# Kernel tuning notes

Hardware: AMD Instinct MI355X
Metric: run time of the kernel (lower is better)

The kernel has to match this reference:

```python
import jax, jax.numpy as jnp
import numpy as np

N = 100000
E = 1000000
F_NODE = 64
F_EDGE = 32
H = 128
C_NODE = 12
C_EDGE = 4


def _glorot(key, shape):
    fan_in, fan_out = shape[0], shape[1]
    s = (6.0 / (fan_in + fan_out)) ** 0.5
    return jax.random.uniform(key, shape, jnp.float32, -s, s)


def setup_inputs() -> dict:
    key = jax.random.key(0)
    ks = jax.random.split(key, 16)
    x = jax.random.normal(ks[0], (N, F_NODE), jnp.float32)
    edge_index = jax.random.randint(ks[1], (2, E), 0, N, jnp.int32)
    edge_attr = jax.random.normal(ks[2], (E, F_EDGE), jnp.float32)
    return {
        "x": x,
        "edge_index": edge_index,
        "edge_attr": edge_attr,
        "We": _glorot(ks[3], (F_NODE, H)), "be": jnp.zeros((H,), jnp.float32),
        "Wc1": _glorot(ks[4], (H, H)), "bc1": jnp.zeros((H,), jnp.float32),
        "Wc2": _glorot(ks[5], (H, H)), "bc2": jnp.zeros((H,), jnp.float32),
        "Wn1": _glorot(ks[6], (H, H // 2)), "bn1": jnp.zeros((H // 2,), jnp.float32),
        "Wn2": _glorot(ks[7], (H // 2, C_NODE)), "bn2": jnp.zeros((C_NODE,), jnp.float32),
        "Wedge1": _glorot(ks[8], (2 * H + F_EDGE, H)), "bedge1": jnp.zeros((H,), jnp.float32),
        "Wedge2": _glorot(ks[9], (H, C_EDGE)), "bedge2": jnp.zeros((C_EDGE,), jnp.float32),
    }


def _gcn_conv(x, W, b, src, tgt, n):
    # PyG GCNConv: add self-loops, symmetric deg normalization, scatter-add.
    xw = x @ W  # [N, H]
    loop = jnp.arange(n, dtype=src.dtype)
    s = jnp.concatenate([src, loop])
    t = jnp.concatenate([tgt, loop])
    deg = jax.ops.segment_sum(jnp.ones_like(t, jnp.float32), t, num_segments=n)
    dinv = jnp.where(deg > 0, jax.lax.rsqrt(jnp.maximum(deg, 1.0)), 0.0)
    norm = dinv[s] * dinv[t]  # [E+N]
    msg = xw[s] * norm[:, None]
    return jax.ops.segment_sum(msg, t, num_segments=n) + b


def reference(x, edge_index, edge_attr, We, be, Wc1, bc1, Wc2, bc2,
              Wn1, bn1, Wn2, bn2, Wedge1, bedge1, Wedge2, bedge2):
    n = x.shape[0]
    row, col = edge_index[0], edge_index[1]
    h = jax.nn.relu(x @ We + be)          # node_embed Linear+ReLU
    h = jax.nn.relu(h)                     # extra F.relu in forward
    h = jax.nn.relu(_gcn_conv(h, Wc1, bc1, row, col, n))
    h = jax.nn.relu(_gcn_conv(h, Wc2, bc2, row, col, n))
    node_logits = jax.nn.relu(h @ Wn1 + bn1) @ Wn2 + bn2
    e = jnp.concatenate([h[row], h[col], edge_attr], axis=-1)  # [E, 2H+Fe]
    edge_logits = jax.nn.relu(e @ Wedge1 + bedge1) @ Wedge2 + bedge2
    return (node_logits, edge_logits)
```

## Files before the change

kernel.cpp:

```cpp
#include <hip/hip_runtime.h>

#define N_NODES 100000
#define N_EDGES 1000000
#define NB_SCAN 391
#define EDGE_OUT_BASE 1200000

typedef __attribute__((ext_vector_type(8))) short short8;
typedef __attribute__((ext_vector_type(4))) unsigned short us4;
typedef __attribute__((ext_vector_type(4))) float f32x4;

__device__ __forceinline__ float bf2f(unsigned short u) {
    unsigned int x = ((unsigned int)u) << 16;
    return __builtin_bit_cast(float, x);
}
__device__ __forceinline__ float lo_bf(unsigned int u) {
    return __builtin_bit_cast(float, u << 16);
}
__device__ __forceinline__ float hi_bf(unsigned int u) {
    return __builtin_bit_cast(float, u & 0xffff0000u);
}
__device__ __forceinline__ unsigned short f2bf(float f) {
    unsigned int x = __builtin_bit_cast(unsigned int, f);
    return (unsigned short)((x + 0x7fffu + ((x >> 16) & 1u)) >> 16);
}

__global__ __launch_bounds__(256) void k_detect(const unsigned short* __restrict__ xr,
                                                int* __restrict__ flag) {
    __shared__ int s[256];
    int t = threadIdx.x;
    int cnt = 0;
    for (int i = t; i < 8192; i += 256) {
        int e = (xr[i] >> 7) & 0xFF;
        if (e >= 148) cnt++;
    }
    s[t] = cnt;
    __syncthreads();
    for (int off = 128; off > 0; off >>= 1) {
        if (t < off) s[t] += s[t + off];
        __syncthreads();
    }
    if (t == 0) *flag = (s[0] > 100) ? 1 : 0;
}

struct WPack { const void* p[14]; };
#define W_TOTAL 87888
__global__ __launch_bounds__(256) void k_convw(WPack wp, const int* __restrict__ flag,
                                               unsigned short* __restrict__ dst) {
    const int starts[15] = {0, 8192, 8320, 24704, 24832, 41216, 41344, 49536,
                            49600, 50368, 50380, 87244, 87372, 87884, 87888};
    bool f32 = (*flag != 0);
    int i = blockIdx.x * 256 + threadIdx.x;
    if (i >= W_TOTAL) return;
    int s = 0;
#pragma unroll
    for (int k = 1; k < 14; k++) s += (i >= starts[k]) ? 1 : 0;
    int j = i - starts[s];
    dst[i] = f32 ? f2bf(((const float*)wp.p[s])[j]) : ((const unsigned short*)wp.p[s])[j];
}
#define OW_We 0
#define OW_be 8192
#define OW_Wc1 8320
#define OW_bc1 24704
#define OW_Wc2 24832
#define OW_bc2 41216
#define OW_Wn1 41344
#define OW_bn1 49536
#define OW_Wn2 49600
#define OW_bn2 50368
#define OW_We1 50380
#define OW_be1 87244
#define OW_We2 87372
#define OW_be2 87884

__global__ __launch_bounds__(256) void k_hist(const int* __restrict__ ecol, int* __restrict__ deg) {
    int e = blockIdx.x * 256 + threadIdx.x;
    if (e < N_EDGES) atomicAdd(&deg[ecol[e]], 1);
}

__global__ __launch_bounds__(256) void k_scanA(const int* __restrict__ deg, int* __restrict__ bsum) {
    __shared__ int s[256];
    int i = blockIdx.x * 256 + threadIdx.x;
    s[threadIdx.x] = (i < N_NODES) ? deg[i] : 0;
    __syncthreads();
    for (int off = 128; off > 0; off >>= 1) {
        if (threadIdx.x < off) s[threadIdx.x] += s[threadIdx.x + off];
        __syncthreads();
    }
    if (threadIdx.x == 0) bsum[blockIdx.x] = s[0];
}

__global__ __launch_bounds__(512) void k_scanB(int* __restrict__ bsum) {
    __shared__ int s[512];
    int t = threadIdx.x;
    int v = (t < NB_SCAN) ? bsum[t] : 0;
    s[t] = v;
    __syncthreads();
    for (int off = 1; off < 512; off <<= 1) {
        int x = (t >= off) ? s[t - off] : 0;
        __syncthreads();
        s[t] += x;
        __syncthreads();
    }
    if (t < NB_SCAN) bsum[t] = s[t] - v;
}

__global__ __launch_bounds__(256) void k_scanC(const int* __restrict__ deg, const int* __restrict__ bsum,
                                               int* __restrict__ row_off, int* __restrict__ cursor,
                                               float* __restrict__ dinv) {
    __shared__ int s[256];
    int i = blockIdx.x * 256 + threadIdx.x;
    int t = threadIdx.x;
    int v = (i < N_NODES) ? deg[i] : 0;
    s[t] = v;
    __syncthreads();
    for (int off = 1; off < 256; off <<= 1) {
        int x = (t >= off) ? s[t - off] : 0;
        __syncthreads();
        s[t] += x;
        __syncthreads();
    }
    int excl = s[t] - v + bsum[blockIdx.x];
    if (i < N_NODES) {
        row_off[i] = excl;
        cursor[i] = excl;
        dinv[i] = rsqrtf((float)(v + 1));
    }
    if (i == N_NODES - 1) row_off[N_NODES] = excl + v;
}

__global__ __launch_bounds__(256) void k_fill(const int* __restrict__ erow, const int* __restrict__ ecol,
                                              int* __restrict__ cursor, int* __restrict__ csr) {
    int e = blockIdx.x * 256 + threadIdx.x;
    if (e < N_EDGES) {
        int pos = atomicAdd(&cursor[ecol[e]], 1);
        csr[pos] = erow[e];
    }
}

template <int K, int O, bool RELU, bool BIAS, bool SCALE>
__global__ __launch_bounds__(256) void gemm_rows(const void* __restrict__ A, int M,
                                                 const unsigned short* __restrict__ W, int o_real,
                                                 const unsigned short* __restrict__ bias,
                                                 void* __restrict__ Out, int out_pitch,
                                                 const float* __restrict__ rowscale,
                                                 const int* aflag, const int* oflag) {
    constexpr int KP = K + 8;
    constexpr int KS = K / 32;
    constexpr int OT = O / 16;
    __shared__ short wt[O * KP];
    __shared__ float bias_s[O];
    int tid = threadIdx.x;
    for (int idx = tid; idx < K * O; idx += 256) {
        int k = idx / O, o = idx % O;
        short w = 0;
        if (o < o_real) w = (short)W[(size_t)k * o_real + o];
        wt[o * KP + k] = w;
    }
    if (BIAS) {
        for (int o = tid; o < O; o += 256) bias_s[o] = (o < o_real) ? bf2f(bias[o]) : 0.f;
    }
    __syncthreads();

    bool af32 = aflag && (*aflag != 0);
    bool of32 = oflag && (*oflag != 0);

    int wid = tid >> 6, lane = tid & 63;
    int rbase = (blockIdx.x * 4 + wid) * 32;
    if (rbase >= M) return;
    int lq = lane >> 4, lr = lane & 15;

    short8 a[2][KS];
#pragma unroll
    for (int rg = 0; rg < 2; rg++) {
        int row = rbase + rg * 16 + lr;
        if (row >= M) row = M - 1;
        if (af32) {
            const float* ap = (const float*)A + (size_t)row * K + lq * 8;
#pragma unroll
            for (int ks = 0; ks < KS; ks++) {
                f32x4 u0 = *(const f32x4*)(ap + ks * 32);
                f32x4 u1 = *(const f32x4*)(ap + ks * 32 + 4);
                short8 v;
                v[0] = (short)f2bf(u0[0]); v[1] = (short)f2bf(u0[1]);
                v[2] = (short)f2bf(u0[2]); v[3] = (short)f2bf(u0[3]);
                v[4] = (short)f2bf(u1[0]); v[5] = (short)f2bf(u1[1]);
                v[6] = (short)f2bf(u1[2]); v[7] = (short)f2bf(u1[3]);
                a[rg][ks] = v;
            }
        } else {
            const unsigned short* ap = (const unsigned short*)A + (size_t)row * K + lq * 8;
#pragma unroll
            for (int ks = 0; ks < KS; ks++) a[rg][ks] = *(const short8*)(ap + ks * 32);
        }
    }

    f32x4 acc[2][OT];
#pragma unroll
    for (int rg = 0; rg < 2; rg++)
#pragma unroll
        for (int j = 0; j < OT; j++) {
            acc[rg][j][0] = 0.f; acc[rg][j][1] = 0.f; acc[rg][j][2] = 0.f; acc[rg][j][3] = 0.f;
        }

#pragma unroll
    for (int j = 0; j < OT; j++) {
        short8 b[KS];
#pragma unroll
        for (int ks = 0; ks < KS; ks++)
            b[ks] = *(const short8*)(&wt[(lr + 16 * j) * KP + ks * 32 + lq * 8]);
#pragma unroll
        for (int rg = 0; rg < 2; rg++)
#pragma unroll
            for (int ks = 0; ks < KS; ks++)
                acc[rg][j] = __builtin_amdgcn_mfma_f32_16x16x32_bf16(a[rg][ks], b[ks], acc[rg][j], 0, 0, 0);
    }

#pragma unroll
    for (int rg = 0; rg < 2; rg++)
#pragma unroll
        for (int j = 0; j < OT; j++)
#pragma unroll
            for (int r = 0; r < 4; r++) {
                int row = rbase + rg * 16 + lq * 4 + r;
                int col = lr + 16 * j;
                if (row < M && col < o_real) {
                    float v = acc[rg][j][r];
                    if (BIAS) v += bias_s[col];
                    if (RELU) v = fmaxf(v, 0.f);
                    if (SCALE) v *= rowscale[row];
                    size_t oi = (size_t)row * out_pitch + col;
                    if (of32) ((float*)Out)[oi] = v;
                    else ((unsigned short*)Out)[oi] = f2bf(v);
                }
            }
}

__global__ __launch_bounds__(256) void gemm_pq(const unsigned short* __restrict__ A, int M,
                                               const unsigned short* __restrict__ W1,
                                               const unsigned short* __restrict__ W2,
                                               unsigned short* __restrict__ Pout,
                                               unsigned short* __restrict__ Qout) {
    __shared__ short wt[128 * 136];
    int tid = threadIdx.x;
    int wid = tid >> 6, lane = tid & 63;
    int rbase = (blockIdx.x * 4 + wid) * 32;
    int lq = lane >> 4, lr = lane & 15;

    short8 a[2][4];
#pragma unroll
    for (int rg = 0; rg < 2; rg++) {
        int row = rbase + rg * 16 + lr;
        if (row >= M) row = M - 1;
        const unsigned short* ap = A + (size_t)row * 128 + lq * 8;
#pragma unroll
        for (int ks = 0; ks < 4; ks++) a[rg][ks] = *(const short8*)(ap + ks * 32);
    }

    for (int idx = tid; idx < 128 * 128; idx += 256) {
        int k = idx >> 7, o = idx & 127;
        wt[o * 136 + k] = (short)W1[idx];
    }
    __syncthreads();
    {
        f32x4 acc[2][8];
#pragma unroll
        for (int rg = 0; rg < 2; rg++)
#pragma unroll
            for (int j = 0; j < 8; j++) {
                acc[rg][j][0] = 0.f; acc[rg][j][1] = 0.f; acc[rg][j][2] = 0.f; acc[rg][j][3] = 0.f;
            }
#pragma unroll
        for (int j = 0; j < 8; j++) {
            short8 b[4];
#pragma unroll
            for (int ks = 0; ks < 4; ks++)
                b[ks] = *(const short8*)(&wt[(lr + 16 * j) * 136 + ks * 32 + lq * 8]);
#pragma unroll
            for (int rg = 0; rg < 2; rg++)
#pragma unroll
                for (int ks = 0; ks < 4; ks++)
                    acc[rg][j] = __builtin_amdgcn_mfma_f32_16x16x32_bf16(a[rg][ks], b[ks], acc[rg][j], 0, 0, 0);
        }
#pragma unroll
        for (int rg = 0; rg < 2; rg++)
#pragma unroll
            for (int j = 0; j < 8; j++)
#pragma unroll
                for (int r = 0; r < 4; r++) {
                    int row = rbase + rg * 16 + lq * 4 + r;
                    if (row < M) Pout[(size_t)row * 128 + lr + 16 * j] = f2bf(acc[rg][j][r]);
                }
    }
    __syncthreads();

    for (int idx = tid; idx < 128 * 128; idx += 256) {
        int k = idx >> 7, o = idx & 127;
        wt[o * 136 + k] = (short)W2[idx];
    }
    __syncthreads();
    {
        f32x4 acc[2][8];
#pragma unroll
        for (int rg = 0; rg < 2; rg++)
#pragma unroll
            for (int j = 0; j < 8; j++) {
                acc[rg][j][0] = 0.f; acc[rg][j][1] = 0.f; acc[rg][j][2] = 0.f; acc[rg][j][3] = 0.f;
            }
#pragma unroll
        for (int j = 0; j < 8; j++) {
            short8 b[4];
#pragma unroll
            for (int ks = 0; ks < 4; ks++)
                b[ks] = *(const short8*)(&wt[(lr + 16 * j) * 136 + ks * 32 + lq * 8]);
#pragma unroll
            for (int rg = 0; rg < 2; rg++)
#pragma unroll
                for (int ks = 0; ks < 4; ks++)
                    acc[rg][j] = __builtin_amdgcn_mfma_f32_16x16x32_bf16(a[rg][ks], b[ks], acc[rg][j], 0, 0, 0);
        }
#pragma unroll
        for (int rg = 0; rg < 2; rg++)
#pragma unroll
            for (int j = 0; j < 8; j++)
#pragma unroll
                for (int r = 0; r < 4; r++) {
                    int row = rbase + rg * 16 + lq * 4 + r;
                    if (row < M) Qout[(size_t)row * 128 + lr + 16 * j] = f2bf(acc[rg][j][r]);
                }
    }
}

__global__ __launch_bounds__(256) void conv_kernel(const unsigned short* __restrict__ xw_s,
                                                   const int* __restrict__ csr_src,
                                                   const int* __restrict__ row_off,
                                                   const float* __restrict__ dinv,
                                                   const unsigned short* __restrict__ bias,
                                                   unsigned short* __restrict__ out) {
    int wid = threadIdx.x >> 6, lane = threadIdx.x & 63;
    int t = blockIdx.x * 4 + wid;
    int beg = row_off[t], end = row_off[t + 1];
    float dt = dinv[t];
    unsigned int v = *(const unsigned int*)(xw_s + (size_t)t * 128 + lane * 2);
    unsigned int bv = *(const unsigned int*)(bias + lane * 2);
    float a0 = lo_bf(v), a1 = hi_bf(v);
    int i = beg;
    for (; i + 4 <= end; i += 4) {
        int s0 = csr_src[i], s1 = csr_src[i + 1], s2 = csr_src[i + 2], s3 = csr_src[i + 3];
        unsigned int u0 = *(const unsigned int*)(xw_s + (size_t)s0 * 128 + lane * 2);
        unsigned int u1 = *(const unsigned int*)(xw_s + (size_t)s1 * 128 + lane * 2);
        unsigned int u2 = *(const unsigned int*)(xw_s + (size_t)s2 * 128 + lane * 2);
        unsigned int u3 = *(const unsigned int*)(xw_s + (size_t)s3 * 128 + lane * 2);
        a0 += lo_bf(u0) + lo_bf(u1) + lo_bf(u2) + lo_bf(u3);
        a1 += hi_bf(u0) + hi_bf(u1) + hi_bf(u2) + hi_bf(u3);
    }
    for (; i < end; i++) {
        int s = csr_src[i];
        unsigned int u = *(const unsigned int*)(xw_s + (size_t)s * 128 + lane * 2);
        a0 += lo_bf(u);
        a1 += hi_bf(u);
    }
    a0 = fmaxf(fmaf(a0, dt, lo_bf(bv)), 0.f);
    a1 = fmaxf(fmaf(a1, dt, hi_bf(bv)), 0.f);
    unsigned int o = (unsigned int)f2bf(a0) | ((unsigned int)f2bf(a1) << 16);
    *(unsigned int*)(out + (size_t)t * 128 + lane * 2) = o;
}

__global__ __launch_bounds__(256) void edge_head(const void* __restrict__ ea,
                                                 const int* __restrict__ erow, const int* __restrict__ ecol,
                                                 const unsigned short* __restrict__ P,
                                                 const unsigned short* __restrict__ Q,
                                                 const unsigned short* __restrict__ wbuf,
                                                 void* __restrict__ out, const int* dtflag) {
    __shared__ short wct[128 * 40];
    __shared__ float w2s[128 * 4];
    __shared__ float b1s[128];
    int tid = threadIdx.x;
    const unsigned short* Wc3 = wbuf + OW_We1 + 256 * 128;
    for (int idx = tid; idx < 32 * 128; idx += 256) {
        int k = idx >> 7, o = idx & 127;
        wct[o * 40 + k] = (short)Wc3[idx];
    }
    for (int idx = tid; idx < 512; idx += 256) w2s[idx] = bf2f(wbuf[OW_We2 + idx]);
    if (tid < 128) b1s[tid] = bf2f(wbuf[OW_be1 + tid]);
    __syncthreads();

    bool f32io = (*dtflag != 0);
    int wid = tid >> 6, lane = tid & 63;
    int e0 = (blockIdx.x * 4 + wid) * 16;
    int lq = lane >> 4, lr = lane & 15;

    short8 efrag;
    if (f32io) {
        const float* eap = (const float*)ea + (size_t)(e0 + lr) * 32 + lq * 8;
        f32x4 u0 = *(const f32x4*)eap;
        f32x4 u1 = *(const f32x4*)(eap + 4);
        efrag[0] = (short)f2bf(u0[0]); efrag[1] = (short)f2bf(u0[1]);
        efrag[2] = (short)f2bf(u0[2]); efrag[3] = (short)f2bf(u0[3]);
        efrag[4] = (short)f2bf(u1[0]); efrag[5] = (short)f2bf(u1[1]);
        efrag[6] = (short)f2bf(u1[2]); efrag[7] = (short)f2bf(u1[3]);
    } else {
        efrag = *(const short8*)((const unsigned short*)ea + (size_t)(e0 + lr) * 32 + lq * 8);
    }

    f32x4 zero; zero[0] = 0.f; zero[1] = 0.f; zero[2] = 0.f; zero[3] = 0.f;
    f32x4 acc[8];
#pragma unroll
    for (int j = 0; j < 8; j++) {
        short8 wfrag = *(const short8*)(&wct[(16 * j + lr) * 40 + lq * 8]);
        acc[j] = __builtin_amdgcn_mfma_f32_16x16x32_bf16(wfrag, efrag, zero, 0, 0, 0);
    }

    int ge = e0 + lr;
    int rn = erow[ge], cn = ecol[ge];
    const unsigned short* Pp = P + (size_t)rn * 128 + lq * 4;
    const unsigned short* Qp = Q + (size_t)cn * 128 + lq * 4;
    f32x4 ov; ov[0] = 0.f; ov[1] = 0.f; ov[2] = 0.f; ov[3] = 0.f;
#pragma unroll
    for (int j = 0; j < 8; j++) {
        int chb = 16 * j + 4 * lq;
        us4 pv = *(const us4*)(Pp + 16 * j);
        us4 qv = *(const us4*)(Qp + 16 * j);
        f32x4 b1v = *(const f32x4*)(&b1s[chb]);
#pragma unroll
        for (int r = 0; r < 4; r++) {
            float t = acc[j][r] + bf2f(pv[r]) + bf2f(qv[r]) + b1v[r];
            t = fmaxf(t, 0.f);
            f32x4 w2v = *(const f32x4*)(&w2s[(chb + r) * 4]);
            ov[0] = fmaf(t, w2v[0], ov[0]);
            ov[1] = fmaf(t, w2v[1], ov[1]);
            ov[2] = fmaf(t, w2v[2], ov[2]);
            ov[3] = fmaf(t, w2v[3], ov[3]);
        }
    }
#pragma unroll
    for (int c = 0; c < 4; c++) {
        ov[c] += __shfl_xor(ov[c], 16);
        ov[c] += __shfl_xor(ov[c], 32);
    }
    if (lq == 0) {
        size_t oi = (size_t)EDGE_OUT_BASE + (size_t)ge * 4;
        if (f32io) {
            f32x4 res;
#pragma unroll
            for (int c = 0; c < 4; c++) res[c] = ov[c] + bf2f(wbuf[OW_be2 + c]);
            *(f32x4*)((float*)out + oi) = res;
        } else {
            us4 res;
#pragma unroll
            for (int c = 0; c < 4; c++) res[c] = f2bf(ov[c] + bf2f(wbuf[OW_be2 + c]));
            *(us4*)((unsigned short*)out + oi) = res;
        }
    }
}

extern "C" void kernel_launch(void* const* d_in, const int* in_sizes, int n_in,
                              void* d_out, int out_size, void* d_ws, size_t ws_size,
                              hipStream_t stream) {
    const void* x = d_in[0];
    const int* ei = (const int*)d_in[1];
    const void* ea = d_in[2];
    const int* erow = ei;
    const int* ecol = ei + N_EDGES;

    char* ws = (char*)d_ws;
    size_t off = 0;
    auto alloc = [&](size_t bytes) -> void* {
        void* p = ws + off;
        off += (bytes + 255) & ~(size_t)255;
        return p;
    };
    unsigned short* Abuf = (unsigned short*)alloc((size_t)N_NODES * 128 * 2);
    unsigned short* Bbuf = (unsigned short*)alloc((size_t)N_NODES * 128 * 2);
    int* deg = (int*)alloc((size_t)N_NODES * 4);
    int* row_off = (int*)alloc((size_t)(N_NODES + 1) * 4);
    int* cursor = (int*)alloc((size_t)N_NODES * 4);
    int* csr = (int*)alloc((size_t)N_EDGES * 4);
    int* bsum = (int*)alloc(512 * 4);
    float* dinv = (float*)alloc((size_t)N_NODES * 4);
    unsigned short* wbuf = (unsigned short*)alloc((size_t)W_TOTAL * 2);
    int* dtflag = (int*)alloc(256);

    k_detect<<<1, 256, 0, stream>>>((const unsigned short*)x, dtflag);

    WPack wp;
    for (int i = 0; i < 14; i++) wp.p[i] = d_in[3 + i];
    k_convw<<<(W_TOTAL + 255) / 256, 256, 0, stream>>>(wp, dtflag, wbuf);

    (void)hipMemsetAsync(deg, 0, (size_t)N_NODES * 4, stream);
    k_hist<<<(N_EDGES + 255) / 256, 256, 0, stream>>>(ecol, deg);
    k_scanA<<<NB_SCAN, 256, 0, stream>>>(deg, bsum);
    k_scanB<<<1, 512, 0, stream>>>(bsum);
    k_scanC<<<NB_SCAN, 256, 0, stream>>>(deg, bsum, row_off, cursor, dinv);
    k_fill<<<(N_EDGES + 255) / 256, 256, 0, stream>>>(erow, ecol, cursor, csr);

    int gB = (N_NODES + 127) / 128;
    gemm_rows<64, 128, true, true, false><<<gB, 256, 0, stream>>>(x, N_NODES, wbuf + OW_We, 128, wbuf + OW_be, Abuf, 128, nullptr, dtflag, nullptr);
    gemm_rows<128, 128, false, false, true><<<gB, 256, 0, stream>>>(Abuf, N_NODES, wbuf + OW_Wc1, 128, nullptr, Bbuf, 128, dinv, nullptr, nullptr);
    conv_kernel<<<N_NODES / 4, 256, 0, stream>>>(Bbuf, csr, row_off, dinv, wbuf + OW_bc1, Abuf);
    gemm_rows<128, 128, false, false, true><<<gB, 256, 0, stream>>>(Abuf, N_NODES, wbuf + OW_Wc2, 128, nullptr, Bbuf, 128, dinv, nullptr, nullptr);
    conv_kernel<<<N_NODES / 4, 256, 0, stream>>>(Bbuf, csr, row_off, dinv, wbuf + OW_bc2, Abuf);
    gemm_rows<128, 64, true, true, false><<<gB, 256, 0, stream>>>(Abuf, N_NODES, wbuf + OW_Wn1, 64, wbuf + OW_bn1, Bbuf, 64, nullptr, nullptr, nullptr);
    gemm_rows<64, 16, false, true, false><<<gB, 256, 0, stream>>>(Bbuf, N_NODES, wbuf + OW_Wn2, 12, wbuf + OW_bn2, d_out, 12, nullptr, nullptr, dtflag);
    gemm_pq<<<gB, 256, 0, stream>>>(Abuf, N_NODES, wbuf + OW_We1, wbuf + OW_We1 + 128 * 128, Bbuf, Abuf);
    edge_head<<<N_EDGES / 64, 256, 0, stream>>>(ea, erow, ecol, Bbuf, Abuf, wbuf, d_out, dtflag);
}
```

Before: 592.9 us.

## Permute P/Q column layout for vector loads; process two rows per wave in conv and edge head

gemm_pq now writes P and Q with permuted columns so each lane of edge_head can fetch 32 contiguous channels with 16-byte loads instead of scattered 8-byte loads. The b1 and W2 tables in shared memory are permuted to match. conv_kernel has each wave aggregate two target nodes at once, and edge_head has each wave handle two 16-edge tiles, so more independent gathers are in flight. This raises register pressure and adds tail-loop code. The interleaved walk over two rows with unequal degrees may also leave lanes idle.

```diff
diff --git a/kernel.cpp b/kernel.cpp
--- a/kernel.cpp
+++ b/kernel.cpp
@@ -256,6 +256,8 @@
         for (int ks = 0; ks < 4; ks++) a[rg][ks] = *(const short8*)(ap + ks * 32);
     }
 
+    int pc0 = (lr >> 2) * 32 + (lr & 3);
+
     for (int idx = tid; idx < 128 * 128; idx += 256) {
         int k = idx >> 7, o = idx & 127;
         wt[o * 136 + k] = (short)W1[idx];
@@ -288,7 +290,7 @@
 #pragma unroll
                 for (int r = 0; r < 4; r++) {
                     int row = rbase + rg * 16 + lq * 4 + r;
-                    if (row < M) Pout[(size_t)row * 128 + lr + 16 * j] = f2bf(acc[rg][j][r]);
+                    if (row < M) Pout[(size_t)row * 128 + pc0 + j * 4] = f2bf(acc[rg][j][r]);
                 }
     }
     __syncthreads();
@@ -325,7 +327,7 @@
 #pragma unroll
                 for (int r = 0; r < 4; r++) {
                     int row = rbase + rg * 16 + lq * 4 + r;
-                    if (row < M) Qout[(size_t)row * 128 + lr + 16 * j] = f2bf(acc[rg][j][r]);
+                    if (row < M) Qout[(size_t)row * 128 + pc0 + j * 4] = f2bf(acc[rg][j][r]);
                 }
     }
 }
@@ -337,32 +339,70 @@
                                                    const unsigned short* __restrict__ bias,
                                                    unsigned short* __restrict__ out) {
     int wid = threadIdx.x >> 6, lane = threadIdx.x & 63;
-    int t = blockIdx.x * 4 + wid;
-    int beg = row_off[t], end = row_off[t + 1];
-    float dt = dinv[t];
-    unsigned int v = *(const unsigned int*)(xw_s + (size_t)t * 128 + lane * 2);
+    int base = (blockIdx.x * 4 + wid) * 2;
+    int t0 = base, t1 = base + 1;
+    int beg0 = row_off[t0], end0 = row_off[t0 + 1];
+    int beg1 = row_off[t1], end1 = row_off[t1 + 1];
+    float dt0 = dinv[t0], dt1 = dinv[t1];
+    unsigned int v0 = *(const unsigned int*)(xw_s + (size_t)t0 * 128 + lane * 2);
+    unsigned int v1 = *(const unsigned int*)(xw_s + (size_t)t1 * 128 + lane * 2);
     unsigned int bv = *(const unsigned int*)(bias + lane * 2);
-    float a0 = lo_bf(v), a1 = hi_bf(v);
-    int i = beg;
-    for (; i + 4 <= end; i += 4) {
-        int s0 = csr_src[i], s1 = csr_src[i + 1], s2 = csr_src[i + 2], s3 = csr_src[i + 3];
+    float a00 = lo_bf(v0), a01 = hi_bf(v0);
+    float a10 = lo_bf(v1), a11 = hi_bf(v1);
+    int i0 = beg0, i1 = beg1;
+    while (i0 + 4 <= end0 && i1 + 4 <= end1) {
+        int s00 = csr_src[i0], s01 = csr_src[i0 + 1], s02 = csr_src[i0 + 2], s03 = csr_src[i0 + 3];
+        int s10 = csr_src[i1], s11 = csr_src[i1 + 1], s12 = csr_src[i1 + 2], s13 = csr_src[i1 + 3];
+        unsigned int u00 = *(const unsigned int*)(xw_s + (size_t)s00 * 128 + lane * 2);
+        unsigned int u01 = *(const unsigned int*)(xw_s + (size_t)s01 * 128 + lane * 2);
+        unsigned int u02 = *(const unsigned int*)(xw_s + (size_t)s02 * 128 + lane * 2);
+        unsigned int u03 = *(const unsigned int*)(xw_s + (size_t)s03 * 128 + lane * 2);
+        unsigned int u10 = *(const unsigned int*)(xw_s + (size_t)s10 * 128 + lane * 2);
+        unsigned int u11 = *(const unsigned int*)(xw_s + (size_t)s11 * 128 + lane * 2);
+        unsigned int u12 = *(const unsigned int*)(xw_s + (size_t)s12 * 128 + lane * 2);
+        unsigned int u13 = *(const unsigned int*)(xw_s + (size_t)s13 * 128 + lane * 2);
+        a00 += lo_bf(u00) + lo_bf(u01) + lo_bf(u02) + lo_bf(u03);
+        a01 += hi_bf(u00) + hi_bf(u01) + hi_bf(u02) + hi_bf(u03);
+        a10 += lo_bf(u10) + lo_bf(u11) + lo_bf(u12) + lo_bf(u13);
+        a11 += hi_bf(u10) + hi_bf(u11) + hi_bf(u12) + hi_bf(u13);
+        i0 += 4; i1 += 4;
+    }
+    for (; i0 + 4 <= end0; i0 += 4) {
+        int s0 = csr_src[i0], s1 = csr_src[i0 + 1], s2 = csr_src[i0 + 2], s3 = csr_src[i0 + 3];
         unsigned int u0 = *(const unsigned int*)(xw_s + (size_t)s0 * 128 + lane * 2);
         unsigned int u1 = *(const unsigned int*)(xw_s + (size_t)s1 * 128 + lane * 2);
         unsigned int u2 = *(const unsigned int*)(xw_s + (size_t)s2 * 128 + lane * 2);
         unsigned int u3 = *(const unsigned int*)(xw_s + (size_t)s3 * 128 + lane * 2);
-        a0 += lo_bf(u0) + lo_bf(u1) + lo_bf(u2) + lo_bf(u3);
-        a1 += hi_bf(u0) + hi_bf(u1) + hi_bf(u2) + hi_bf(u3);
-    }
-    for (; i < end; i++) {
-        int s = csr_src[i];
+        a00 += lo_bf(u0) + lo_bf(u1) + lo_bf(u2) + lo_bf(u3);
+        a01 += hi_bf(u0) + hi_bf(u1) + hi_bf(u2) + hi_bf(u3);
+    }
+    for (; i1 + 4 <= end1; i1 += 4) {
+        int s0 = csr_src[i1], s1 = csr_src[i1 + 1], s2 = csr_src[i1 + 2], s3 = csr_src[i1 + 3];
+        unsigned int u0 = *(const unsigned int*)(xw_s + (size_t)s0 * 128 + lane * 2);
+        unsigned int u1 = *(const unsigned int*)(xw_s + (size_t)s1 * 128 + lane * 2);
+        unsigned int u2 = *(const unsigned int*)(xw_s + (size_t)s2 * 128 + lane * 2);
+        unsigned int u3 = *(const unsigned int*)(xw_s + (size_t)s3 * 128 + lane * 2);
+        a10 += lo_bf(u0) + lo_bf(u1) + lo_bf(u2) + lo_bf(u3);
+        a11 += hi_bf(u0) + hi_bf(u1) + hi_bf(u2) + hi_bf(u3);
+    }
+    for (; i0 < end0; i0++) {
+        int s = csr_src[i0];
         unsigned int u = *(const unsigned int*)(xw_s + (size_t)s * 128 + lane * 2);
-        a0 += lo_bf(u);
-        a1 += hi_bf(u);
-    }
-    a0 = fmaxf(fmaf(a0, dt, lo_bf(bv)), 0.f);
-    a1 = fmaxf(fmaf(a1, dt, hi_bf(bv)), 0.f);
-    unsigned int o = (unsigned int)f2bf(a0) | ((unsigned int)f2bf(a1) << 16);
-    *(unsigned int*)(out + (size_t)t * 128 + lane * 2) = o;
+        a00 += lo_bf(u); a01 += hi_bf(u);
+    }
+    for (; i1 < end1; i1++) {
+        int s = csr_src[i1];
+        unsigned int u = *(const unsigned int*)(xw_s + (size_t)s * 128 + lane * 2);
+        a10 += lo_bf(u); a11 += hi_bf(u);
+    }
+    a00 = fmaxf(fmaf(a00, dt0, lo_bf(bv)), 0.f);
+    a01 = fmaxf(fmaf(a01, dt0, hi_bf(bv)), 0.f);
+    a10 = fmaxf(fmaf(a10, dt1, lo_bf(bv)), 0.f);
+    a11 = fmaxf(fmaf(a11, dt1, hi_bf(bv)), 0.f);
+    unsigned int o0 = (unsigned int)f2bf(a00) | ((unsigned int)f2bf(a01) << 16);
+    unsigned int o1 = (unsigned int)f2bf(a10) | ((unsigned int)f2bf(a11) << 16);
+    *(unsigned int*)(out + (size_t)t0 * 128 + lane * 2) = o0;
+    *(unsigned int*)(out + (size_t)t1 * 128 + lane * 2) = o1;
 }
 
 __global__ __launch_bounds__(256) void edge_head(const void* __restrict__ ea,
@@ -380,75 +420,129 @@
         int k = idx >> 7, o = idx & 127;
         wct[o * 40 + k] = (short)Wc3[idx];
     }
-    for (int idx = tid; idx < 512; idx += 256) w2s[idx] = bf2f(wbuf[OW_We2 + idx]);
-    if (tid < 128) b1s[tid] = bf2f(wbuf[OW_be1 + tid]);
+    for (int idx = tid; idx < 512; idx += 256) {
+        int p = idx >> 2, o = idx & 3;
+        int ch = 16 * ((p & 31) >> 2) + 4 * (p >> 5) + (p & 3);
+        w2s[idx] = bf2f(wbuf[OW_We2 + ch * 4 + o]);
+    }
+    if (tid < 128) {
+        int p = tid;
+        int ch = 16 * ((p & 31) >> 2) + 4 * (p >> 5) + (p & 3);
+        b1s[p] = bf2f(wbuf[OW_be1 + ch]);
+    }
     __syncthreads();
 
     bool f32io = (*dtflag != 0);
     int wid = tid >> 6, lane = tid & 63;
-    int e0 = (blockIdx.x * 4 + wid) * 16;
     int lq = lane >> 4, lr = lane & 15;
-
-    short8 efrag;
-    if (f32io) {
-        const float* eap = (const float*)ea + (size_t)(e0 + lr) * 32 + lq * 8;
-        f32x4 u0 = *(const f32x4*)eap;
-        f32x4 u1 = *(const f32x4*)(eap + 4);
-        efrag[0] = (short)f2bf(u0[0]); efrag[1] = (short)f2bf(u0[1]);
-        efrag[2] = (short)f2bf(u0[2]); efrag[3] = (short)f2bf(u0[3]);
-        efrag[4] = (short)f2bf(u1[0]); efrag[5] = (short)f2bf(u1[1]);
-        efrag[6] = (short)f2bf(u1[2]); efrag[7] = (short)f2bf(u1[3]);
-    } else {
-        efrag = *(const short8*)((const unsigned short*)ea + (size_t)(e0 + lr) * 32 + lq * 8);
-    }
+    int tbase = (blockIdx.x * 4 + wid) * 2;
+    int e0a = tbase * 16, e0b = e0a + 16;
+
+    int gea = e0a + lr, geb = e0b + lr;
+    bool va = gea < N_EDGES, vb = geb < N_EDGES;
+    int geca = va ? gea : (N_EDGES - 1);
+    int gecb = vb ? geb : (N_EDGES - 1);
+
+    int rna = erow[geca], cna = ecol[geca];
+    int rnb = erow[gecb], cnb = ecol[gecb];
+
+    auto load_efrag = [&](int ge) -> short8 {
+        short8 v;
+        if (f32io) {
+            const float* eap = (const float*)ea + (size_t)ge * 32 + lq * 8;
+            f32x4 u0 = *(const f32x4*)eap;
+            f32x4 u1 = *(const f32x4*)(eap + 4);
+            v[0] = (short)f2bf(u0[0]); v[1] = (short)f2bf(u0[1]);
+            v[2] = (short)f2bf(u0[2]); v[3] = (short)f2bf(u0[3]);
+            v[4] = (short)f2bf(u1[0]); v[5] = (short)f2bf(u1[1]);
+            v[6] = (short)f2bf(u1[2]); v[7] = (short)f2bf(u1[3]);
+        } else {
+            v = *(const short8*)((const unsigned short*)ea + (size_t)ge * 32 + lq * 8);
+        }
+        return v;
+    };
+    short8 efA = load_efrag(geca);
+    short8 efB = load_efrag(gecb);
 
     f32x4 zero; zero[0] = 0.f; zero[1] = 0.f; zero[2] = 0.f; zero[3] = 0.f;
-    f32x4 acc[8];
+    f32x4 accA[8], accB[8];
 #pragma unroll
     for (int j = 0; j < 8; j++) {
         short8 wfrag = *(const short8*)(&wct[(16 * j + lr) * 40 + lq * 8]);
-        acc[j] = __builtin_amdgcn_mfma_f32_16x16x32_bf16(wfrag, efrag, zero, 0, 0, 0);
-    }
-
-    int ge = e0 + lr;
-    int rn = erow[ge], cn = ecol[ge];
-    const unsigned short* Pp = P + (size_t)rn * 128 + lq * 4;
-    const unsigned short* Qp = Q + (size_t)cn * 128 + lq * 4;
-    f32x4 ov; ov[0] = 0.f; ov[1] = 0.f; ov[2] = 0.f; ov[3] = 0.f;
-#pragma unroll
-    for (int j = 0; j < 8; j++) {
-        int chb = 16 * j + 4 * lq;
-        us4 pv = *(const us4*)(Pp + 16 * j);
-        us4 qv = *(const us4*)(Qp + 16 * j);
-        f32x4 b1v = *(const f32x4*)(&b1s[chb]);
-#pragma unroll
-        for (int r = 0; r < 4; r++) {
-            float t = acc[j][r] + bf2f(pv[r]) + bf2f(qv[r]) + b1v[r];
-            t = fmaxf(t, 0.f);
-            f32x4 w2v = *(const f32x4*)(&w2s[(chb + r) * 4]);
-            ov[0] = fmaf(t, w2v[0], ov[0]);
-            ov[1] = fmaf(t, w2v[1], ov[1]);
-            ov[2] = fmaf(t, w2v[2], ov[2]);
-            ov[3] = fmaf(t, w2v[3], ov[3]);
-        }
-    }
+        accA[j] = __builtin_amdgcn_mfma_f32_16x16x32_bf16(wfrag, efA, zero, 0, 0, 0);
+        accB[j] = __builtin_amdgcn_mfma_f32_16x16x32_bf16(wfrag, efB, zero, 0, 0, 0);
+    }
+
+    const unsigned short* PpA = P + (size_t)rna * 128 + lq * 32;
+    const unsigned short* QpA = Q + (size_t)cna * 128 + lq * 32;
+    const unsigned short* PpB = P + (size_t)rnb * 128 + lq * 32;
+    const unsigned short* QpB = Q + (size_t)cnb * 128 + lq * 32;
+    f32x4 ovA, ovB;
+    ovA[0] = 0.f; ovA[1] = 0.f; ovA[2] = 0.f; ovA[3] = 0.f;
+    ovB[0] = 0.f; ovB[1] = 0.f; ovB[2] = 0.f; ovB[3] = 0.f;
 #pragma unroll
     for (int c = 0; c < 4; c++) {
-        ov[c] += __shfl_xor(ov[c], 16);
-        ov[c] += __shfl_xor(ov[c], 32);
+        short8 pvA = *(const short8*)(PpA + c * 8);
+        short8 qvA = *(const short8*)(QpA + c * 8);
+        short8 pvB = *(const short8*)(PpB + c * 8);
+        short8 qvB = *(const short8*)(QpB + c * 8);
+        int pbase = lq * 32 + c * 8;
+#pragma unroll
+        for (int jj = 0; jj < 2; jj++) {
+            int j = 2 * c + jj;
+#pragma unroll
+            for (int r = 0; r < 4; r++) {
+                int idx = jj * 4 + r;
+                float b1v = b1s[pbase + idx];
+                f32x4 w2v = *(const f32x4*)(&w2s[(pbase + idx) * 4]);
+                float tA = accA[j][r] + bf2f((unsigned short)pvA[idx]) + bf2f((unsigned short)qvA[idx]) + b1v;
+                tA = fmaxf(tA, 0.f);
+                ovA[0] = fmaf(tA, w2v[0], ovA[0]);
+                ovA[1] = fmaf(tA, w2v[1], ovA[1]);
+                ovA[2] = fmaf(tA, w2v[2], ovA[2]);
+                ovA[3] = fmaf(tA, w2v[3], ovA[3]);
+                float tB = accB[j][r] + bf2f((unsigned short)pvB[idx]) + bf2f((unsigned short)qvB[idx]) + b1v;
+                tB = fmaxf(tB, 0.f);
+                ovB[0] = fmaf(tB, w2v[0], ovB[0]);
+                ovB[1] = fmaf(tB, w2v[1], ovB[1]);
+                ovB[2] = fmaf(tB, w2v[2], ovB[2]);
+                ovB[3] = fmaf(tB, w2v[3], ovB[3]);
+            }
+        }
+    }
+#pragma unroll
+    for (int c = 0; c < 4; c++) {
+        ovA[c] += __shfl_xor(ovA[c], 16);
+        ovA[c] += __shfl_xor(ovA[c], 32);
+        ovB[c] += __shfl_xor(ovB[c], 16);
+        ovB[c] += __shfl_xor(ovB[c], 32);
     }
     if (lq == 0) {
-        size_t oi = (size_t)EDGE_OUT_BASE + (size_t)ge * 4;
-        if (f32io) {
-            f32x4 res;
-#pragma unroll
-            for (int c = 0; c < 4; c++) res[c] = ov[c] + bf2f(wbuf[OW_be2 + c]);
-            *(f32x4*)((float*)out + oi) = res;
-        } else {
-            us4 res;
-#pragma unroll
-            for (int c = 0; c < 4; c++) res[c] = f2bf(ov[c] + bf2f(wbuf[OW_be2 + c]));
-            *(us4*)((unsigned short*)out + oi) = res;
+        float be2_0 = bf2f(wbuf[OW_be2 + 0]), be2_1 = bf2f(wbuf[OW_be2 + 1]);
+        float be2_2 = bf2f(wbuf[OW_be2 + 2]), be2_3 = bf2f(wbuf[OW_be2 + 3]);
+        if (va) {
+            size_t oi = (size_t)EDGE_OUT_BASE + (size_t)gea * 4;
+            if (f32io) {
+                f32x4 res; res[0] = ovA[0] + be2_0; res[1] = ovA[1] + be2_1;
+                res[2] = ovA[2] + be2_2; res[3] = ovA[3] + be2_3;
+                *(f32x4*)((float*)out + oi) = res;
+            } else {
+                us4 res; res[0] = f2bf(ovA[0] + be2_0); res[1] = f2bf(ovA[1] + be2_1);
+                res[2] = f2bf(ovA[2] + be2_2); res[3] = f2bf(ovA[3] + be2_3);
+                *(us4*)((unsigned short*)out + oi) = res;
+            }
+        }
+        if (vb) {
+            size_t oi = (size_t)EDGE_OUT_BASE + (size_t)geb * 4;
+            if (f32io) {
+                f32x4 res; res[0] = ovB[0] + be2_0; res[1] = ovB[1] + be2_1;
+                res[2] = ovB[2] + be2_2; res[3] = ovB[3] + be2_3;
+                *(f32x4*)((float*)out + oi) = res;
+            } else {
+                us4 res; res[0] = f2bf(ovB[0] + be2_0); res[1] = f2bf(ovB[1] + be2_1);
+                res[2] = f2bf(ovB[2] + be2_2); res[3] = f2bf(ovB[3] + be2_3);
+                *(us4*)((unsigned short*)out + oi) = res;
+            }
         }
     }
 }
@@ -496,11 +590,11 @@
     int gB = (N_NODES + 127) / 128;
     gemm_rows<64, 128, true, true, false><<<gB, 256, 0, stream>>>(x, N_NODES, wbuf + OW_We, 128, wbuf + OW_be, Abuf, 128, nullptr, dtflag, nullptr);
     gemm_rows<128, 128, false, false, true><<<gB, 256, 0, stream>>>(Abuf, N_NODES, wbuf + OW_Wc1, 128, nullptr, Bbuf, 128, dinv, nullptr, nullptr);
-    conv_kernel<<<N_NODES / 4, 256, 0, stream>>>(Bbuf, csr, row_off, dinv, wbuf + OW_bc1, Abuf);
+    conv_kernel<<<N_NODES / 8, 256, 0, stream>>>(Bbuf, csr, row_off, dinv, wbuf + OW_bc1, Abuf);
     gemm_rows<128, 128, false, false, true><<<gB, 256, 0, stream>>>(Abuf, N_NODES, wbuf + OW_Wc2, 128, nullptr, Bbuf, 128, dinv, nullptr, nullptr);
-    conv_kernel<<<N_NODES / 4, 256, 0, stream>>>(Bbuf, csr, row_off, dinv, wbuf + OW_bc2, Abuf);
+    conv_kernel<<<N_NODES / 8, 256, 0, stream>>>(Bbuf, csr, row_off, dinv, wbuf + OW_bc2, Abuf);
     gemm_rows<128, 64, true, true, false><<<gB, 256, 0, stream>>>(Abuf, N_NODES, wbuf + OW_Wn1, 64, wbuf + OW_bn1, Bbuf, 64, nullptr, nullptr, nullptr);
     gemm_rows<64, 16, false, true, false><<<gB, 256, 0, stream>>>(Bbuf, N_NODES, wbuf + OW_Wn2, 12, wbuf + OW_bn2, d_out, 12, nullptr, nullptr, dtflag);
     gemm_pq<<<gB, 256, 0, stream>>>(Abuf, N_NODES, wbuf + OW_We1, wbuf + OW_We1 + 128 * 128, Bbuf, Abuf);
-    edge_head<<<N_EDGES / 64, 256, 0, stream>>>(ea, erow, ecol, Bbuf, Abuf, wbuf, d_out, dtflag);
-}
+    edge_head<<<(N_EDGES + 127) / 128, 256, 0, stream>>>(ea, erow, ecol, Bbuf, Abuf, wbuf, d_out, dtflag);
+}
```

New measurement: 559.5 us. 1.06x faster.
